# Optimization experiments

Measured on AMD Instinct MI355X. Metric: run time of the kernel, lower is better.

Reference implementation:

```python
import math
import jax, jax.numpy as jnp
import numpy as np

D_MODEL = 768
EXPAND = 2
D_INNER = EXPAND * D_MODEL  # 1536
D_STATE = 16
D_CONV = 4
DT_RANK = math.ceil(D_INNER / 16)  # 96
B, L = 2, 2048
LN_EPS = 1e-5


def setup_inputs() -> dict:
    key = jax.random.key(0)
    ks = jax.random.split(key, 10)
    x = jax.random.normal(ks[0], (B, L, D_MODEL), dtype=jnp.float32)
    ln_g = jnp.ones((D_MODEL,), jnp.float32)
    ln_b = jnp.zeros((D_MODEL,), jnp.float32)
    W_in = jax.random.normal(ks[1], (D_MODEL, 2 * D_INNER), jnp.float32) / np.sqrt(D_MODEL)
    conv_w = jax.random.normal(ks[2], (D_INNER, 1, D_CONV), jnp.float32) / np.sqrt(D_CONV)
    conv_b = jax.random.normal(ks[3], (D_INNER,), jnp.float32) * 0.02
    W_xproj = jax.random.normal(ks[4], (D_INNER, DT_RANK + 2 * D_STATE), jnp.float32) / np.sqrt(D_INNER)
    W_dt = jax.random.normal(ks[5], (DT_RANK, D_INNER), jnp.float32) / np.sqrt(DT_RANK)
    # dt bias init: inverse-softplus of dt ~ LogUniform(1e-3, 1e-1)
    dt = jnp.exp(jax.random.uniform(ks[6], (D_INNER,)) * (math.log(0.1) - math.log(0.001)) + math.log(0.001))
    b_dt = dt + jnp.log(-jnp.expm1(-dt))
    log_A = jnp.log(jnp.tile(jnp.arange(1, D_STATE + 1, dtype=jnp.float32), (D_INNER, 1)))  # (d_inner, N)
    D_param = jnp.ones((D_INNER,), jnp.float32)
    W_out = jax.random.normal(ks[7], (D_INNER, D_MODEL), jnp.float32) / np.sqrt(D_INNER)
    return dict(x=x, ln_g=ln_g, ln_b=ln_b, W_in=W_in, conv_w=conv_w, conv_b=conv_b,
                W_xproj=W_xproj, W_dt=W_dt, b_dt=b_dt, log_A=log_A, D_param=D_param, W_out=W_out)


def _mamba_block(x, ln_g, ln_b, W_in, conv_w, conv_b, W_xproj, W_dt, b_dt, log_A, D_param, W_out):
    residual = x
    # LayerNorm
    mu = jnp.mean(x, axis=-1, keepdims=True)
    var = jnp.var(x, axis=-1, keepdims=True)
    xn = (x - mu) * jax.lax.rsqrt(var + LN_EPS) * ln_g + ln_b
    # in projection -> (u, v)
    uv = xn @ W_in  # (B, L, 2*d_inner)
    u, v = jnp.split(uv, 2, axis=-1)
    # causal depthwise conv1d along length (torch pads both sides then truncates -> left pad only)
    u_c = jnp.transpose(u, (0, 2, 1))  # (B, d_inner, L)
    u_c = jax.lax.conv_general_dilated(
        u_c, conv_w, window_strides=(1,), padding=[(D_CONV - 1, 0)],
        dimension_numbers=('NCH', 'OIH', 'NCH'), feature_group_count=D_INNER)
    u_c = u_c + conv_b[None, :, None]
    u = jnp.transpose(u_c, (0, 2, 1))  # (B, L, d_inner)
    u = jax.nn.silu(u)
    # Selective SSM
    x_dbl = u @ W_xproj  # (B, L, dt_rank + 2N)
    dlt, Bm, Cm = jnp.split(x_dbl, [DT_RANK, DT_RANK + D_STATE], axis=-1)
    delta = jax.nn.softplus(dlt @ W_dt + b_dt)  # (B, L, d_inner)
    A = -jnp.exp(log_A)  # (d_inner, N)
    A_bar = jnp.exp(jnp.einsum('bld,dn->bldn', delta, A))         # discretized A
    Bu = jnp.einsum('bld,bln,bld->bldn', delta, Bm, u)            # B_bar * u
    # parallel scan: h_k = A_bar_k * h_{k-1} + Bu_k
    def comb(e1, e2):
        a1, b1 = e1
        a2, b2 = e2
        return a1 * a2, a2 * b1 + b2
    _, h = jax.lax.associative_scan(comb, (A_bar, Bu), axis=1)
    y = jnp.einsum('bldn,bln->bld', h, Cm) + u * D_param
    # gate + residual
    y = y * jax.nn.silu(v)
    return y @ W_out + residual


def reference(x, ln_g, ln_b, W_in, conv_w, conv_b, W_xproj, W_dt, b_dt, log_A, D_param, W_out):
    return _mamba_block(x, ln_g, ln_b, W_in, conv_w, conv_b, W_xproj, W_dt, b_dt, log_A, D_param, W_out)
```

## Files before the change

### kernel.cpp

```cpp
#include <hip/hip_runtime.h>

#define D_MODEL 768
#define D_INNER 1536
#define D_STATE 16
#define DT_RANK 96
#define BB 2
#define LL 2048
#define TT (BB*LL)
#define NC 64
#define CL 32
#define LOG2E 1.44269504f

typedef unsigned short u16;
typedef short bf16x8 __attribute__((ext_vector_type(8)));
typedef unsigned short u16x8 __attribute__((ext_vector_type(8)));
typedef float f32x4  __attribute__((ext_vector_type(4)));

__device__ __forceinline__ float bf2f(u16 u) {
    union { unsigned int i; float f; } c; c.i = ((unsigned int)u) << 16; return c.f;
}
__device__ __forceinline__ u16 f2bf(float f) {
    union { float f; unsigned int i; } c; c.f = f;
    unsigned int x = c.i;
    return (u16)((x + 0x7fffu + ((x >> 16) & 1u)) >> 16);
}
__device__ __forceinline__ float bfu_lo(unsigned int u) {
    union { unsigned int i; float f; } c; c.i = u << 16; return c.f;
}
__device__ __forceinline__ float bfu_hi(unsigned int u) {
    union { unsigned int i; float f; } c; c.i = u & 0xFFFF0000u; return c.f;
}
__device__ __forceinline__ float ldx(const void* p, size_t i, bool f32) {
    return f32 ? ((const float*)p)[i] : bf2f(((const u16*)p)[i]);
}

__device__ __forceinline__ void gload16(const u16* g, u16* l) {
    __builtin_amdgcn_global_load_lds(
        (const __attribute__((address_space(1))) unsigned int*)g,
        (__attribute__((address_space(3))) unsigned int*)l, 16, 0, 0);
}

__device__ __forceinline__ void xcd_swz(int& bx, int& by) {
    const int gx = gridDim.x;
    const int cpx = (gx * gridDim.y) >> 3;
    const int bid = by * gx + bx;
    const int w = (bid & 7) * cpx + (bid >> 3);
    bx = w % gx; by = w / gx;
}

__global__ __launch_bounds__(256) void prep_kernel(
    const void* __restrict__ W_in, const void* __restrict__ W_xp,
    const void* __restrict__ W_dt, const void* __restrict__ W_out,
    u16* __restrict__ WtIn, u16* __restrict__ WtXp,
    u16* __restrict__ WtDt, u16* __restrict__ WtOut,
    const void* __restrict__ x, const void* __restrict__ g,
    const void* __restrict__ b, u16* __restrict__ xn,
    int* __restrict__ flagw)
{
    const int t = threadIdx.x;
    __shared__ int sbad;
    if (t == 0) sbad = 0;
    __syncthreads();
    {
        const u16* px = (const u16*)x;
        int bad = 0;
        for (int i = t; i < 2048; i += 256)
            if (!(fabsf(bf2f(px[2 * i])) < 1e4f)) bad = 1;
        if (bad) atomicOr(&sbad, 1);
    }
    __syncthreads();
    const bool f32 = (sbad != 0);
    int bid = blockIdx.x;
    if (bid == 0 && t == 0) *flagw = sbad;
    if (bid >= 960) {
        const int tok = bid - 960;
        const size_t base = (size_t)tok * D_MODEL;
        float v[3];
        v[0] = ldx(x, base + t, f32);
        v[1] = ldx(x, base + t + 256, f32);
        v[2] = ldx(x, base + t + 512, f32);
        float s = v[0] + v[1] + v[2];
        float q = v[0]*v[0] + v[1]*v[1] + v[2]*v[2];
        #pragma unroll
        for (int o = 32; o > 0; o >>= 1) {
            s += __shfl_down(s, o, 64);
            q += __shfl_down(q, o, 64);
        }
        __shared__ float ss[4], qq[4];
        if ((t & 63) == 0) { ss[t >> 6] = s; qq[t >> 6] = q; }
        __syncthreads();
        const float S = ss[0] + ss[1] + ss[2] + ss[3];
        const float Q = qq[0] + qq[1] + qq[2] + qq[3];
        const float mu  = S * (1.f / D_MODEL);
        const float var = Q * (1.f / D_MODEL) - mu * mu;
        const float rs  = rsqrtf(var + 1e-5f);
        u16* outr = xn + base;
        #pragma unroll
        for (int i = 0; i < 3; ++i) {
            const int c = t + i * 256;
            outr[c] = f2bf((v[i] - mu) * rs * ldx(g, c, f32) + ldx(b, c, f32));
        }
        return;
    }
    const void* src; u16* dst; int K, N, bx, by;
    if (bid < 576)      { src = W_in;  dst = WtIn;  K = 768;  N = 3072; bx = bid % 48; by = bid / 48; }
    else if (bid < 624) { bid -= 576; src = W_xp;  dst = WtXp;  K = 1536; N = 128;  bx = bid % 2;  by = bid / 2; }
    else if (bid < 672) { bid -= 624; src = W_dt;  dst = WtDt;  K = 96;   N = 1536; bx = bid % 24; by = bid / 24; }
    else                { bid -= 672; src = W_out; dst = WtOut; K = 1536; N = 768;  bx = bid % 12; by = bid / 12; }
    __shared__ u16 tile[64][72];
    const int n0 = bx * 64, k0 = by * 64;
    {
        const int r = t >> 2, c = (t & 3) * 16;
        const int k = k0 + r;
        if (k < K) {
            if (f32) {
                const float* sp = (const float*)src + (size_t)k * N + n0 + c;
                #pragma unroll
                for (int q = 0; q < 4; ++q) {
                    const float4 v = *(const float4*)(sp + 4 * q);
                    tile[r][c + 4*q + 0] = f2bf(v.x);
                    tile[r][c + 4*q + 1] = f2bf(v.y);
                    tile[r][c + 4*q + 2] = f2bf(v.z);
                    tile[r][c + 4*q + 3] = f2bf(v.w);
                }
            } else {
                const u16* sp = (const u16*)src + (size_t)k * N + n0 + c;
                *(u16x8*)(&tile[r][c])     = *(const u16x8*)(sp);
                *(u16x8*)(&tile[r][c + 8]) = *(const u16x8*)(sp + 8);
            }
        }
    }
    __syncthreads();
    {
        const int nl = t >> 2, kl = (t & 3) * 16;
        const int n = n0 + nl;
        if (k0 + kl < K) {
            u16x8 t0, t1;
            #pragma unroll
            for (int i = 0; i < 8; ++i) t0[i] = tile[kl + i][nl];
            #pragma unroll
            for (int i = 0; i < 8; ++i) t1[i] = tile[kl + 8 + i][nl];
            u16* dp = dst + (size_t)n * K + k0 + kl;
            *(u16x8*)(dp)     = t0;
            *(u16x8*)(dp + 8) = t1;
        }
    }
}

template<int EPI, int BK>
__global__ __launch_bounds__(256) void mfma_gemm(
    const u16* __restrict__ A, const u16* __restrict__ Bt,
    u16* __restrict__ C, void* __restrict__ Cout, const void* __restrict__ aux,
    const int* __restrict__ flagp,
    int Kslice, int lda, int ldbt, int ldc)
{
    const bool f32 = (*flagp != 0);
    __shared__ alignas(16) u16 As[3 * 64 * BK];
    __shared__ alignas(16) u16 Bs[3 * 64 * BK];
    const int tid  = threadIdx.x;
    const int wave = tid >> 6, lane = tid & 63;
    const int lrow = lane & 15, quad = lane >> 4;
    int bx = blockIdx.x, by = blockIdx.y;
    xcd_swz(bx, by);
    const int row0 = by * 64, col0 = bx * 64;
    constexpr int LPR = BK / 8;
    constexpr int PM  = LPR - 1;
    constexpr int RPO = 64 / LPR;
    constexpr int NOP = BK / 32;
    constexpr int V1  = 2 * NOP;
    constexpr int V2  = 4 * NOP;
    const int srow = lane / LPR;
    const int pc   = (lane % LPR) ^ (srow & PM);
    const int skk  = pc * 8;
    const int wb   = wave * 16 * BK;
    const u16* gA = A  + (size_t)(row0 + wave * 16 + srow) * lda  + skk;
    const u16* gB = Bt + (size_t)(col0 + wave * 16 + srow) * ldbt + skk;
    const int nst = Kslice / BK;
    constexpr int BUF = 64 * BK;
    #pragma unroll
    for (int o = 0; o < NOP; ++o) {
        gload16(gA + (size_t)o * RPO * lda,  &As[wb + o * 512]);
        gload16(gB + (size_t)o * RPO * ldbt, &Bs[wb + o * 512]);
    }
    if (nst > 1) {
        #pragma unroll
        for (int o = 0; o < NOP; ++o) {
            gload16(gA + BK + (size_t)o * RPO * lda,  &As[BUF + wb + o * 512]);
            gload16(gB + BK + (size_t)o * RPO * ldbt, &Bs[BUF + wb + o * 512]);
        }
    }
    f32x4 acc[4] = {{0.f,0.f,0.f,0.f},{0.f,0.f,0.f,0.f},{0.f,0.f,0.f,0.f},{0.f,0.f,0.f,0.f}};
    const int sw = (lrow & PM) << 3;
    int cur = 0, nxt2 = 2;
    for (int t = 0; t < nst; ++t) {
        if (t + 2 < nst) {
            const int kt = (t + 2) * BK;
            const int poff = nxt2 * BUF;
            #pragma unroll
            for (int o = 0; o < NOP; ++o) {
                gload16(gA + kt + (size_t)o * RPO * lda,  &As[poff + wb + o * 512]);
                gload16(gB + kt + (size_t)o * RPO * ldbt, &Bs[poff + wb + o * 512]);
            }
            asm volatile("s_waitcnt vmcnt(%0)" :: "i"(V2) : "memory");
        } else if (t + 1 < nst) {
            asm volatile("s_waitcnt vmcnt(%0)" :: "i"(V1) : "memory");
        } else {
            asm volatile("s_waitcnt vmcnt(0)" ::: "memory");
        }
        __builtin_amdgcn_s_barrier();
        asm volatile("" ::: "memory");
        const int boff = cur * BUF;
        #pragma unroll
        for (int kk = 0; kk < NOP; ++kk) {
            const bf16x8 af = *(const bf16x8*)(
                &As[boff + (wave * 16 + lrow) * BK + ((kk * 32 + quad * 8) ^ sw)]);
            #pragma unroll
            for (int q = 0; q < 4; ++q) {
                const bf16x8 bq = *(const bf16x8*)(
                    &Bs[boff + (q * 16 + lrow) * BK + ((kk * 32 + quad * 8) ^ sw)]);
                acc[q] = __builtin_amdgcn_mfma_f32_16x16x32_bf16(af, bq, acc[q], 0, 0, 0);
            }
        }
        __builtin_amdgcn_s_barrier();
        asm volatile("" ::: "memory");
        cur = (cur == 2) ? 0 : cur + 1;
        nxt2 = (nxt2 == 2) ? 0 : nxt2 + 1;
    }
    #pragma unroll
    for (int t = 0; t < 4; ++t) {
        #pragma unroll
        for (int r = 0; r < 4; ++r) {
            const int row = row0 + wave * 16 + quad * 4 + r;
            const int col = col0 + t * 16 + lrow;
            const size_t idx = (size_t)row * ldc + col;
            float vv = acc[t][r];
            if (EPI == 1) {
                vv += ldx(aux, col, f32);
                vv = (vv > 20.f) ? vv : log1pf(__expf(vv));
                C[idx] = f2bf(vv);
            } else if (EPI == 2) {
                vv += ldx(aux, idx, f32);
                if (f32) ((float*)Cout)[idx] = vv;
                else     ((u16*)Cout)[idx]   = f2bf(vv);
            } else {
                C[idx] = f2bf(vv);
            }
        }
    }
}

template<int EPI>
__global__ __launch_bounds__(256) void mfma_gemm128(
    const u16* __restrict__ A, const u16* __restrict__ Bt,
    u16* __restrict__ C, void* __restrict__ Cout, const void* __restrict__ aux,
    const int* __restrict__ flagp,
    int K, int lda, int ldbt, int ldc)
{
    const bool f32 = (*flagp != 0);
    __shared__ alignas(16) u16 As[3 * 128 * 32];
    __shared__ alignas(16) u16 Bs[3 * 128 * 32];
    const int tid  = threadIdx.x;
    const int wave = tid >> 6, lane = tid & 63;
    const int lrow = lane & 15, quad = lane >> 4;
    const int wy = wave >> 1, wx = wave & 1;
    int bx = blockIdx.x, by = blockIdx.y;
    xcd_swz(bx, by);
    const int row0 = by * 128, col0 = bx * 128;
    const int srw = lane >> 2;
    const int pc  = (lane & 3) ^ (srw & 3);
    const int skk = pc * 8;
    const int r0 = wave * 16 + srw;
    const int r1 = r0 + 64;
    const int wb0 = wave * 512, wb1 = (wave + 4) * 512;
    const u16* gA0 = A  + (size_t)(row0 + r0) * lda  + skk;
    const u16* gA1 = A  + (size_t)(row0 + r1) * lda  + skk;
    const u16* gB0 = Bt + (size_t)(col0 + r0) * ldbt + skk;
    const u16* gB1 = Bt + (size_t)(col0 + r1) * ldbt + skk;
    const int nst = K >> 5;
    constexpr int BUF = 128 * 32;
    gload16(gA0, &As[wb0]); gload16(gA1, &As[wb1]);
    gload16(gB0, &Bs[wb0]); gload16(gB1, &Bs[wb1]);
    if (nst > 1) {
        gload16(gA0 + 32, &As[BUF + wb0]); gload16(gA1 + 32, &As[BUF + wb1]);
        gload16(gB0 + 32, &Bs[BUF + wb0]); gload16(gB1 + 32, &Bs[BUF + wb1]);
    }
    f32x4 acc[4][4];
    #pragma unroll
    for (int i = 0; i < 4; ++i)
        #pragma unroll
        for (int j = 0; j < 4; ++j) acc[i][j] = (f32x4){0.f,0.f,0.f,0.f};
    const int sw = (lrow & 3) << 3;
    int cur = 0, nxt2 = 2;
    for (int t = 0; t < nst; ++t) {
        if (t + 2 < nst) {
            const int kt = (t + 2) * 32;
            const int poff = nxt2 * BUF;
            gload16(gA0 + kt, &As[poff + wb0]); gload16(gA1 + kt, &As[poff + wb1]);
            gload16(gB0 + kt, &Bs[poff + wb0]); gload16(gB1 + kt, &Bs[poff + wb1]);
            asm volatile("s_waitcnt vmcnt(8)" ::: "memory");
        } else if (t + 1 < nst) {
            asm volatile("s_waitcnt vmcnt(4)" ::: "memory");
        } else {
            asm volatile("s_waitcnt vmcnt(0)" ::: "memory");
        }
        __builtin_amdgcn_s_barrier();
        asm volatile("" ::: "memory");
        const int boff = cur * BUF;
        bf16x8 af[4], bf_[4];
        #pragma unroll
        for (int i = 0; i < 4; ++i)
            af[i] = *(const bf16x8*)(
                &As[boff + (wy * 64 + i * 16 + lrow) * 32 + ((quad * 8) ^ sw)]);
        #pragma unroll
        for (int j = 0; j < 4; ++j)
            bf_[j] = *(const bf16x8*)(
                &Bs[boff + (wx * 64 + j * 16 + lrow) * 32 + ((quad * 8) ^ sw)]);
        #pragma unroll
        for (int i = 0; i < 4; ++i)
            #pragma unroll
            for (int j = 0; j < 4; ++j)
                acc[i][j] = __builtin_amdgcn_mfma_f32_16x16x32_bf16(af[i], bf_[j], acc[i][j], 0, 0, 0);
        __builtin_amdgcn_s_barrier();
        asm volatile("" ::: "memory");
        cur = (cur == 2) ? 0 : cur + 1;
        nxt2 = (nxt2 == 2) ? 0 : nxt2 + 1;
    }
    #pragma unroll
    for (int i = 0; i < 4; ++i) {
        #pragma unroll
        for (int j = 0; j < 4; ++j) {
            #pragma unroll
            for (int r = 0; r < 4; ++r) {
                const int row = row0 + wy * 64 + i * 16 + quad * 4 + r;
                const int col = col0 + wx * 64 + j * 16 + lrow;
                const size_t idx = (size_t)row * ldc + col;
                C[idx] = f2bf(acc[i][j][r]);
            }
        }
    }
}

__global__ __launch_bounds__(256) void conv_silu_kernel(
    const u16* __restrict__ uv, const void* __restrict__ cw, const void* __restrict__ cb,
    u16* __restrict__ us, const int* __restrict__ flagp)
{
    const bool f32 = (*flagp != 0);
    const int gid = blockIdx.x * 256 + threadIdx.x;
    const int nd8 = D_INNER / 8;
    const int d8  = gid % nd8;
    const int tok = gid / nd8;
    const int d   = d8 * 8;
    const int l   = tok & (LL - 1);
    float acc[8], w[4][8];
    #pragma unroll
    for (int i = 0; i < 8; ++i) acc[i] = ldx(cb, d + i, f32);
    #pragma unroll
    for (int i = 0; i < 8; ++i) {
        if (f32) {
            const float4 wv = *(const float4*)((const float*)cw + (size_t)(d + i) * 4);
            w[0][i] = wv.x; w[1][i] = wv.y; w[2][i] = wv.z; w[3][i] = wv.w;
        } else {
            const u16* wp = (const u16*)cw + (size_t)(d + i) * 4;
            w[0][i] = bf2f(wp[0]); w[1][i] = bf2f(wp[1]);
            w[2][i] = bf2f(wp[2]); w[3][i] = bf2f(wp[3]);
        }
    }
    #pragma unroll
    for (int j = 0; j < 4; ++j) {
        if (l - 3 + j >= 0) {
            const u16x8 uvv = *(const u16x8*)(&uv[(size_t)(tok - 3 + j) * (2 * D_INNER) + d]);
            #pragma unroll
            for (int i = 0; i < 8; ++i) acc[i] += bf2f(uvv[i]) * w[j][i];
        }
    }
    u16x8 o;
    #pragma unroll
    for (int i = 0; i < 8; ++i) o[i] = f2bf(acc[i] / (1.f + __expf(-acc[i])));
    *(u16x8*)(&us[(size_t)tok * D_INNER + d]) = o;
}

__global__ __launch_bounds__(256) void scan1_kernel(
    const u16* __restrict__ delta, const u16* __restrict__ us,
    const u16* __restrict__ xdbl, const void* __restrict__ log_A,
    float* __restrict__ carrySD, float* __restrict__ carryH,
    const int* __restrict__ flagp)
{
    const bool f32 = (*flagp != 0);
    const int d = blockIdx.x * 256 + threadIdx.x;
    const int c = blockIdx.y, b = blockIdx.z;
    float A2[16], h[16];
    #pragma unroll
    for (int j = 0; j < 16; ++j) {
        A2[j] = -__expf(ldx(log_A, d * D_STATE + j, f32)) * LOG2E;
        h[j] = 0.f;
    }
    bool pw = true;
    #pragma unroll
    for (int j = 1; j < 16; ++j)
        pw = pw && (fabsf(A2[j] - (j + 1) * A2[0]) <= 0.02f * (j + 1) * fabsf(A2[0]));
    float sdl = 0.f;
    size_t tok = (size_t)b * LL + c * CL;
    if (pw) {
        #pragma unroll 2
        for (int t = 0; t < CL; ++t, ++tok) {
            const float dl = bf2f(delta[tok * D_INNER + d]);
            const float ul = bf2f(us[tok * D_INNER + d]);
            const uint4 B0 = *(const uint4*)(xdbl + tok * 128 + DT_RANK);
            const uint4 B1 = *(const uint4*)(xdbl + tok * 128 + DT_RANK + 8);
            const float dlul = dl * ul;
            sdl += dl;
            const unsigned int bw[8] = {B0.x,B0.y,B0.z,B0.w,B1.x,B1.y,B1.z,B1.w};
            const float a1 = exp2f(dl * A2[0]);
            float aj = 1.f;
            #pragma unroll
            for (int j = 0; j < 16; ++j) {
                aj *= a1;
                const float Bn = (j & 1) ? bfu_hi(bw[j >> 1]) : bfu_lo(bw[j >> 1]);
                h[j] = aj * h[j] + dlul * Bn;
            }
        }
    } else {
        #pragma unroll 2
        for (int t = 0; t < CL; ++t, ++tok) {
            const float dl = bf2f(delta[tok * D_INNER + d]);
            const float ul = bf2f(us[tok * D_INNER + d]);
            const uint4 B0 = *(const uint4*)(xdbl + tok * 128 + DT_RANK);
            const uint4 B1 = *(const uint4*)(xdbl + tok * 128 + DT_RANK + 8);
            const float dlul = dl * ul;
            sdl += dl;
            const unsigned int bw[8] = {B0.x,B0.y,B0.z,B0.w,B1.x,B1.y,B1.z,B1.w};
            #pragma unroll
            for (int j = 0; j < 16; ++j) {
                const float Bn = (j & 1) ? bfu_hi(bw[j >> 1]) : bfu_lo(bw[j >> 1]);
                h[j] = exp2f(dl * A2[j]) * h[j] + dlul * Bn;
            }
        }
    }
    const size_t cc = (size_t)b * NC + c;
    carrySD[cc * D_INNER + d] = sdl;
    const size_t ci = cc * (D_INNER * D_STATE) + d;
    #pragma unroll
    for (int j = 0; j < 16; ++j)
        carryH[ci + (size_t)j * D_INNER] = h[j];
}

__global__ __launch_bounds__(256) void scan3_kernel(
    const u16* __restrict__ delta, const u16* __restrict__ us,
    const u16* __restrict__ xdbl, u16* __restrict__ uv,
    const void* __restrict__ log_A, const void* __restrict__ D_param,
    const float* __restrict__ carrySD, const float* __restrict__ carryH,
    const int* __restrict__ flagp)
{
    const bool f32 = (*flagp != 0);
    const int d = blockIdx.x * 256 + threadIdx.x;
    const int c = blockIdx.y, b = blockIdx.z;
    const float Dd = ldx(D_param, d, f32);
    float A2[16], h[16];
    #pragma unroll
    for (int j = 0; j < 16; ++j) {
        A2[j] = -__expf(ldx(log_A, d * D_STATE + j, f32)) * LOG2E;
        h[j] = 0.f;
    }
    bool pw = true;
    #pragma unroll
    for (int j = 1; j < 16; ++j)
        pw = pw && (fabsf(A2[j] - (j + 1) * A2[0]) <= 0.02f * (j + 1) * fabsf(A2[0]));
    for (int cp = 0; cp < c; ++cp) {
        const size_t cc = (size_t)b * NC + cp;
        const float sdl = carrySD[cc * D_INNER + d];
        const float* hp = carryH + cc * (D_INNER * D_STATE) + d;
        #pragma unroll
        for (int j = 0; j < 16; ++j)
            h[j] = exp2f(A2[j] * sdl) * h[j] + hp[(size_t)j * D_INNER];
    }
    size_t tok = (size_t)b * LL + c * CL;
    if (pw) {
        #pragma unroll 2
        for (int t = 0; t < CL; ++t, ++tok) {
            const float dl = bf2f(delta[tok * D_INNER + d]);
            const float ul = bf2f(us[tok * D_INNER + d]);
            const uint4 B0 = *(const uint4*)(xdbl + tok * 128 + DT_RANK);
            const uint4 B1 = *(const uint4*)(xdbl + tok * 128 + DT_RANK + 8);
            const uint4 C0 = *(const uint4*)(xdbl + tok * 128 + DT_RANK + D_STATE);
            const uint4 C1 = *(const uint4*)(xdbl + tok * 128 + DT_RANK + D_STATE + 8);
            const float dlul = dl * ul;
            const unsigned int bw[8] = {B0.x,B0.y,B0.z,B0.w,B1.x,B1.y,B1.z,B1.w};
            const unsigned int cw_[8] = {C0.x,C0.y,C0.z,C0.w,C1.x,C1.y,C1.z,C1.w};
            const float a1 = exp2f(dl * A2[0]);
            float aj = 1.f, p = 0.f;
            #pragma unroll
            for (int j = 0; j < 16; ++j) {
                aj *= a1;
                const float Bn = (j & 1) ? bfu_hi(bw[j >> 1]) : bfu_lo(bw[j >> 1]);
                const float Cn = (j & 1) ? bfu_hi(cw_[j >> 1]) : bfu_lo(cw_[j >> 1]);
                h[j] = aj * h[j] + dlul * Bn;
                p += h[j] * Cn;
            }
            const float vv = bf2f(uv[tok * (2*D_INNER) + D_INNER + d]);
            uv[tok * (2*D_INNER) + d] = f2bf((p + ul * Dd) * (vv / (1.f + __expf(-vv))));
        }
    } else {
        #pragma unroll 2
        for (int t = 0; t < CL; ++t, ++tok) {
            const float dl = bf2f(delta[tok * D_INNER + d]);
            const float ul = bf2f(us[tok * D_INNER + d]);
            const uint4 B0 = *(const uint4*)(xdbl + tok * 128 + DT_RANK);
            const uint4 B1 = *(const uint4*)(xdbl + tok * 128 + DT_RANK + 8);
            const uint4 C0 = *(const uint4*)(xdbl + tok * 128 + DT_RANK + D_STATE);
            const uint4 C1 = *(const uint4*)(xdbl + tok * 128 + DT_RANK + D_STATE + 8);
            const float dlul = dl * ul;
            const unsigned int bw[8] = {B0.x,B0.y,B0.z,B0.w,B1.x,B1.y,B1.z,B1.w};
            const unsigned int cw_[8] = {C0.x,C0.y,C0.z,C0.w,C1.x,C1.y,C1.z,C1.w};
            float p = 0.f;
            #pragma unroll
            for (int j = 0; j < 16; ++j) {
                const float Bn = (j & 1) ? bfu_hi(bw[j >> 1]) : bfu_lo(bw[j >> 1]);
                const float Cn = (j & 1) ? bfu_hi(cw_[j >> 1]) : bfu_lo(cw_[j >> 1]);
                h[j] = exp2f(dl * A2[j]) * h[j] + dlul * Bn;
                p += h[j] * Cn;
            }
            const float vv = bf2f(uv[tok * (2*D_INNER) + D_INNER + d]);
            uv[tok * (2*D_INNER) + d] = f2bf((p + ul * Dd) * (vv / (1.f + __expf(-vv))));
        }
    }
}

extern "C" void kernel_launch(void* const* d_in, const int* in_sizes, int n_in,
                              void* d_out, int out_size, void* d_ws, size_t ws_size,
                              hipStream_t stream)
{
    const void* x      = d_in[0];
    const void* ln_g   = d_in[1];
    const void* ln_b   = d_in[2];
    const void* W_in   = d_in[3];
    const void* conv_w = d_in[4];
    const void* conv_b = d_in[5];
    const void* W_xp   = d_in[6];
    const void* W_dt   = d_in[7];
    const void* b_dt   = d_in[8];
    const void* log_A  = d_in[9];
    const void* D_par  = d_in[10];
    const void* W_out  = d_in[11];

    int* flag  = (int*)d_ws;
    u16* ws    = (u16*)((char*)d_ws + 512);
    u16* xn    = ws;
    u16* uv    = xn + (size_t)TT * D_MODEL;
    u16* us    = uv + (size_t)TT * 2 * D_INNER;
    u16* xdbl  = us + (size_t)TT * D_INNER;
    u16* delta = xdbl + (size_t)TT * 128;
    float* carryH  = (float*)(delta + (size_t)TT * D_INNER);
    float* carrySD = carryH + (size_t)BB * NC * D_INNER * D_STATE;
    u16* WtIn  = (u16*)(carrySD + (size_t)BB * NC * D_INNER);
    u16* WtXp  = WtIn  + (size_t)2 * D_INNER * D_MODEL;
    u16* WtDt  = WtXp  + (size_t)(DT_RANK + 2 * D_STATE) * D_INNER;
    u16* WtOut = WtDt  + (size_t)D_INNER * DT_RANK;

    prep_kernel<<<960 + TT, 256, 0, stream>>>(
        W_in, W_xp, W_dt, W_out, WtIn, WtXp, WtDt, WtOut,
        x, ln_g, ln_b, xn, flag);
    mfma_gemm128<0><<<dim3(2 * D_INNER / 128, TT / 128), 256, 0, stream>>>(
        xn, WtIn, uv, nullptr, nullptr, flag, D_MODEL, D_MODEL, D_MODEL, 2 * D_INNER);
    conv_silu_kernel<<<(TT * D_INNER / 8) / 256, 256, 0, stream>>>(uv, conv_w, conv_b, us, flag);
    mfma_gemm<0, 64><<<dim3(2, TT / 64, 1), 256, 0, stream>>>(
        us, WtXp, xdbl, nullptr, nullptr, flag,
        D_INNER, D_INNER, D_INNER, 128);
    mfma_gemm<1, 32><<<dim3(D_INNER / 64, TT / 64, 1), 256, 0, stream>>>(
        xdbl, WtDt, delta, nullptr, b_dt, flag,
        DT_RANK, 128, DT_RANK, D_INNER);
    scan1_kernel<<<dim3(D_INNER / 256, NC, BB), 256, 0, stream>>>(
        delta, us, xdbl, log_A, carrySD, carryH, flag);
    scan3_kernel<<<dim3(D_INNER / 256, NC, BB), 256, 0, stream>>>(
        delta, us, xdbl, uv, log_A, D_par, carrySD, carryH, flag);
    mfma_gemm<2, 64><<<dim3(D_MODEL / 64, TT / 64, 1), 256, 0, stream>>>(
        uv, WtOut, nullptr, d_out, x, flag,
        D_INNER, 2 * D_INNER, D_INNER, D_MODEL);
}
```

Measured before the change: 317.7 us.

## Add a separate carry-propagation kernel instead of per-chunk prefix recomputation

Adds a scan2 kernel that sequentially combines chunk carries per (batch, channel, state) and writes each chunk's incoming state in place into carryH. scan3 then loads its initial state directly rather than re-walking all preceding chunks. This removes quadratic-in-chunks redundant exp and load work in scan3, at the cost of one extra kernel launch and a serial 64-step loop per thread.

```diff
diff --git a/kernel.cpp b/kernel.cpp
--- a/kernel.cpp
+++ b/kernel.cpp
@@ -444,35 +444,50 @@
         carryH[ci + (size_t)j * D_INNER] = h[j];
 }
 
+__global__ __launch_bounds__(256) void scan2_kernel(
+    const float* __restrict__ carrySD, float* __restrict__ carryH,
+    const void* __restrict__ log_A, const int* __restrict__ flagp)
+{
+    const bool f32 = (*flagp != 0);
+    const int gid = blockIdx.x * 256 + threadIdx.x;
+    const int b   = gid / (D_INNER * D_STATE);
+    const int dn  = gid % (D_INNER * D_STATE);
+    const int j   = dn / D_INNER, d = dn % D_INNER;
+    const float A2j = -__expf(ldx(log_A, d * D_STATE + j, f32)) * LOG2E;
+    float hrun = 0.f;
+    #pragma unroll 4
+    for (int c = 0; c < NC; ++c) {
+        const size_t cc = (size_t)b * NC + c;
+        const float sdl = carrySD[cc * D_INNER + d];
+        const size_t ci = cc * (D_INNER * D_STATE) + dn;
+        const float hh = carryH[ci];
+        carryH[ci] = hrun;
+        hrun = exp2f(A2j * sdl) * hrun + hh;
+    }
+}
+
 __global__ __launch_bounds__(256) void scan3_kernel(
     const u16* __restrict__ delta, const u16* __restrict__ us,
     const u16* __restrict__ xdbl, u16* __restrict__ uv,
     const void* __restrict__ log_A, const void* __restrict__ D_param,
-    const float* __restrict__ carrySD, const float* __restrict__ carryH,
-    const int* __restrict__ flagp)
+    const float* __restrict__ carryH, const int* __restrict__ flagp)
 {
     const bool f32 = (*flagp != 0);
     const int d = blockIdx.x * 256 + threadIdx.x;
     const int c = blockIdx.y, b = blockIdx.z;
     const float Dd = ldx(D_param, d, f32);
     float A2[16], h[16];
-    #pragma unroll
-    for (int j = 0; j < 16; ++j) {
+    const size_t ci = ((size_t)b * NC + c) * (D_INNER * D_STATE) + d;
+    #pragma unroll
+    for (int j = 0; j < 16; ++j)
         A2[j] = -__expf(ldx(log_A, d * D_STATE + j, f32)) * LOG2E;
-        h[j] = 0.f;
-    }
     bool pw = true;
     #pragma unroll
     for (int j = 1; j < 16; ++j)
         pw = pw && (fabsf(A2[j] - (j + 1) * A2[0]) <= 0.02f * (j + 1) * fabsf(A2[0]));
-    for (int cp = 0; cp < c; ++cp) {
-        const size_t cc = (size_t)b * NC + cp;
-        const float sdl = carrySD[cc * D_INNER + d];
-        const float* hp = carryH + cc * (D_INNER * D_STATE) + d;
-        #pragma unroll
-        for (int j = 0; j < 16; ++j)
-            h[j] = exp2f(A2[j] * sdl) * h[j] + hp[(size_t)j * D_INNER];
-    }
+    #pragma unroll
+    for (int j = 0; j < 16; ++j)
+        h[j] = carryH[ci + (size_t)j * D_INNER];
     size_t tok = (size_t)b * LL + c * CL;
     if (pw) {
         #pragma unroll 2
@@ -570,8 +585,10 @@
         DT_RANK, 128, DT_RANK, D_INNER);
     scan1_kernel<<<dim3(D_INNER / 256, NC, BB), 256, 0, stream>>>(
         delta, us, xdbl, log_A, carrySD, carryH, flag);
+    scan2_kernel<<<(BB * D_INNER * D_STATE) / 256, 256, 0, stream>>>(
+        carrySD, carryH, log_A, flag);
     scan3_kernel<<<dim3(D_INNER / 256, NC, BB), 256, 0, stream>>>(
-        delta, us, xdbl, uv, log_A, D_par, carrySD, carryH, flag);
+        delta, us, xdbl, uv, log_A, D_par, carryH, flag);
     mfma_gemm<2, 64><<<dim3(D_MODEL / 64, TT / 64, 1), 256, 0, stream>>>(
         uv, WtOut, nullptr, d_out, x, flag,
         D_INNER, 2 * D_INNER, D_INNER, D_MODEL);
```

Result: faster. 284.7 us (-10.4%).
